# Performance work log

Measured on AMD Instinct MI355X. Metric: run time of the kernel, lower is better.

Reference implementation:

```python
import jax, jax.numpy as jnp
import numpy as np
from jax import lax

B, C, H, W = 4, 256, 64, 64
C8 = C // 8


def _conv1x1(x, w, b):
    # x: (B,C,H,W), w: (O,C) -> (B,O,H,W)
    return jnp.einsum('bchw,oc->bohw', x, w) + b[None, :, None, None]


def setup_inputs() -> dict:
    key = jax.random.key(0)
    ks = jax.random.split(key, 9)
    s1 = 1.0 / np.sqrt(C)          # fan-in scale for 1x1 convs
    sf = 1.0 / np.sqrt(2 * C * 9)  # fan-in scale for 3x3 conv
    return {
        'front_x':     jax.random.normal(ks[0], (B, C, H, W), jnp.float32),
        'cross_x':     jax.random.normal(ks[1], (B, C, H, W), jnp.float32),
        'front_x_hat': jax.random.normal(ks[2], (B, C, H, W), jnp.float32),
        'Wq': jax.random.normal(ks[3], (C8, C), jnp.float32) * s1,
        'bq': jnp.zeros((C8,), jnp.float32),
        'Wk': jax.random.normal(ks[4], (C8, C), jnp.float32) * s1,
        'bk': jnp.zeros((C8,), jnp.float32),
        'Wv': jax.random.normal(ks[5], (C, C), jnp.float32) * s1,
        'bv': jnp.zeros((C,), jnp.float32),
        'Wf': jax.random.normal(ks[6], (C, 2 * C, 3, 3), jnp.float32) * sf,
        'bf': jnp.zeros((C,), jnp.float32),
    }


def reference(front_x, cross_x, front_x_hat, Wq, bq, Wk, bk, Wv, bv, Wf, bf):
    b, c, h, w = front_x.shape
    hw = h * w
    # projections -> (B, C/8, HW)
    q = _conv1x1(cross_x, Wq, bq).reshape(b, -1, hw)
    k = _conv1x1(front_x, Wk, bk).reshape(b, -1, hw)
    # energy[b,i,j] = <key_i, query_j>  (B, HW, HW)
    energy = jnp.einsum('bci,bcj->bij', k, q)
    front_star = jnp.max(energy, axis=1)     # (B, HW) best key score per query
    front_arg = jnp.argmax(energy, axis=1)   # (B, HW) best key index per query
    # value projection and hard gather of best-matching value per position
    v = _conv1x1(front_x_hat, Wv, bv).reshape(b, c, hw)
    T = jnp.take_along_axis(v, front_arg[:, None, :], axis=2).reshape(b, c, h, w)
    S = front_star.reshape(b, 1, h, w)
    cat = jnp.concatenate([front_x, T], axis=1)  # (B, 2C, H, W)
    res = lax.conv_general_dilated(
        cat, Wf, window_strides=(1, 1), padding='SAME',
        dimension_numbers=('NCHW', 'OIHW', 'NCHW')) + bf[None, :, None, None]
    return front_x + res * S
```

## Files before the change

### kernel.cpp

```cpp
#include <hip/hip_runtime.h>

#define Bn 4
#define Cn 256
#define C8 32
#define Hn 64
#define Wn 64
#define HWn 4096
#define PADR 80
#define ROWS (HWn + 2 * PADR)
#define MARGIN 6e-3f

typedef __bf16 bf16x8 __attribute__((ext_vector_type(8)));
typedef float floatx4 __attribute__((ext_vector_type(4)));
typedef unsigned short u16x8 __attribute__((ext_vector_type(8)));

__device__ __forceinline__ unsigned short f2bf(float f) {
  union { float f; unsigned int u; } c; c.f = f;
  unsigned int u = c.u;
  return (unsigned short)((u + 0x7FFFu + ((u >> 16) & 1u)) >> 16);
}
__device__ __forceinline__ float bf2f(unsigned short h) {
  union { unsigned int u; float f; } c; c.u = ((unsigned int)h) << 16;
  return c.f;
}
__device__ __forceinline__ void gl_lds16(const void* g, void* l) {
  __builtin_amdgcn_global_load_lds(
      (__attribute__((address_space(1))) void*)(uintptr_t)g,
      (__attribute__((address_space(3))) void*)(uintptr_t)l, 16, 0, 0);
}

__global__ void prep_w(const float* __restrict__ Wq, const float* __restrict__ Wk,
                       const float* __restrict__ Wv, const float* __restrict__ Wf,
                       float* __restrict__ Wqf, float* __restrict__ Wkf,
                       unsigned short* __restrict__ Wvb, unsigned short* __restrict__ Wfb,
                       int* __restrict__ cnt) {
  size_t t = (size_t)blockIdx.x * 256 + threadIdx.x;
  if (t == 0) cnt[0] = 0;
  if (t < 8192) {
    int o = (int)(t / 256), c = (int)(t % 256);
    Wqf[(size_t)c * 32 + o] = Wq[t];
    Wkf[(size_t)c * 32 + o] = Wk[t];
  }
  if (t < 65536) Wvb[t] = f2bf(Wv[t]);
  if (t < (size_t)9 * 256 * 512) {
    int tap = (int)(t / (256 * 512));
    int rem = (int)(t % (256 * 512));
    int o = rem / 512, ci = rem % 512;
    Wfb[t] = f2bf(Wf[((size_t)o * 512 + ci) * 9 + tap]);
  }
}

__global__ __launch_bounds__(1024) void proj_qk(
    const float* __restrict__ cross_x, const float* __restrict__ front_x,
    const float* __restrict__ Wqf, const float* __restrict__ bq,
    const float* __restrict__ Wkf, const float* __restrict__ bk,
    float* __restrict__ qf, float* __restrict__ kf,
    unsigned short* __restrict__ qhi, unsigned short* __restrict__ qlo,
    unsigned short* __restrict__ khi, unsigned short* __restrict__ klo) {
  int tid = threadIdx.x;
  int lane = tid & 63, wv = tid >> 6;
  int slice = wv & 3;
  int chunk = wv >> 2;
  int j = blockIdx.x * 64 + lane;
  int b = blockIdx.y;
  int z = blockIdx.z;
  const float* x = (z == 0) ? cross_x : front_x;
  const float* Wg = (z == 0) ? Wqf : Wkf;
  const float* bd = (z == 0) ? bq : bk;
  float* outp = (z == 0) ? qf : kf;
  unsigned short* hip_ = (z == 0) ? qhi : khi;
  unsigned short* lop_ = (z == 0) ? qlo : klo;
  int o0 = slice * 8;
  int c0 = chunk * 64;

  __shared__ __align__(16) float Wl[8192];
  __shared__ float part[3 * 4 * 8 * 64];

  for (int u = tid; u < 8192; u += 1024) Wl[u] = Wg[u];
  __syncthreads();

  const float* xb = x + (size_t)b * Cn * HWn + j;
  floatx4 a0 = (floatx4)0.0f, a1 = (floatx4)0.0f;
#pragma unroll 16
  for (int c = c0; c < c0 + 64; ++c) {
    float xv = xb[(size_t)c * HWn];
    floatx4 wa = *reinterpret_cast<const floatx4*>(&Wl[c * 32 + o0]);
    floatx4 wb = *reinterpret_cast<const floatx4*>(&Wl[c * 32 + o0 + 4]);
    a0 += wa * xv;
    a1 += wb * xv;
  }
  if (chunk > 0) {
    float* dst = &part[(((chunk - 1) * 4 + slice) * 8) * 64];
#pragma unroll
    for (int o = 0; o < 4; ++o) { dst[o * 64 + lane] = a0[o]; dst[(o + 4) * 64 + lane] = a1[o]; }
  }
  __syncthreads();
  if (chunk != 0) return;
#pragma unroll
  for (int q = 0; q < 3; ++q) {
    const float* src = &part[((q * 4 + slice) * 8) * 64];
#pragma unroll
    for (int o = 0; o < 4; ++o) { a0[o] += src[o * 64 + lane]; a1[o] += src[(o + 4) * 64 + lane]; }
  }
  float acc[8];
#pragma unroll
  for (int o = 0; o < 4; ++o) { acc[o] = a0[o] + bd[o0 + o]; acc[o + 4] = a1[o] + bd[o0 + 4 + o]; }

  float* op = outp + ((size_t)b * HWn + j) * C8 + o0;
  u16x8 hv, lv;
#pragma unroll
  for (int o = 0; o < 8; ++o) {
    op[o] = acc[o];
    unsigned short h = f2bf(acc[o]);
    hv[o] = h;
    lv[o] = f2bf(acc[o] - bf2f(h));
  }
  *reinterpret_cast<u16x8*>(hip_ + ((size_t)b * HWn + j) * C8 + o0) = hv;
  *reinterpret_cast<u16x8*>(lop_ + ((size_t)b * HWn + j) * C8 + o0) = lv;
}

__global__ __launch_bounds__(1024) void energy_approx(
    const unsigned short* __restrict__ khi, const unsigned short* __restrict__ klo,
    const unsigned short* __restrict__ qhi, const unsigned short* __restrict__ qlo,
    float* __restrict__ star, int* __restrict__ argb,
    int* __restrict__ cnt, int* __restrict__ list) {
  int b = blockIdx.y;
  int j0 = blockIdx.x * 32;
  int tid = threadIdx.x;
  int lane = tid & 63, wv = tid >> 6;
  int lm = lane & 15, lq = lane >> 4;

  __shared__ float bv1S[16][32];
  __shared__ int   bi1S[16][32];
  __shared__ float bv2S[16][32];

  bf16x8 qh[2], ql[2];
#pragma unroll
  for (int s = 0; s < 2; ++s) {
    int j = j0 + s * 16 + lm;
    qh[s] = *reinterpret_cast<const bf16x8*>(qhi + ((size_t)b * HWn + j) * 32 + lq * 8);
    ql[s] = *reinterpret_cast<const bf16x8*>(qlo + ((size_t)b * HWn + j) * 32 + lq * 8);
  }
  const unsigned short* kh_base = khi + (size_t)b * HWn * 32 + lq * 8;
  const unsigned short* kl_base = klo + (size_t)b * HWn * 32 + lq * 8;

  float b1[2], b2[2];
#pragma unroll
  for (int s = 0; s < 2; ++s) { b1[s] = -3.0e38f; b2[s] = -3.0e38f; }

  int ibase = wv * 256;
#pragma unroll 4
  for (int it = 0; it < 16; ++it) {
    int i0 = ibase + it * 16;
    bf16x8 ah = *reinterpret_cast<const bf16x8*>(kh_base + (size_t)(i0 + lm) * 32);
    bf16x8 al = *reinterpret_cast<const bf16x8*>(kl_base + (size_t)(i0 + lm) * 32);
#pragma unroll
    for (int s = 0; s < 2; ++s) {
      floatx4 acc = (floatx4)0.0f;
      acc = __builtin_amdgcn_mfma_f32_16x16x32_bf16(ah, qh[s], acc, 0, 0, 0);
      acc = __builtin_amdgcn_mfma_f32_16x16x32_bf16(ah, ql[s], acc, 0, 0, 0);
      acc = __builtin_amdgcn_mfma_f32_16x16x32_bf16(al, qh[s], acc, 0, 0, 0);
#pragma unroll
      for (int r = 0; r < 4; ++r) {
        unsigned code = (unsigned)(it * 4 + r);
        union { float f; unsigned u; } cv; cv.f = acc[r];
        cv.u = (cv.u & ~63u) | code;
        float vp = cv.f;
        b2[s] = __builtin_amdgcn_fmed3f(vp, b1[s], b2[s]);
        b1[s] = fmaxf(b1[s], vp);
      }
    }
  }
  int i1[2];
#pragma unroll
  for (int s = 0; s < 2; ++s) {
    union { float f; unsigned u; } cv; cv.f = b1[s];
    unsigned code = cv.u & 63u;
    i1[s] = ibase + (int)(code >> 2) * 16 + lq * 4 + (int)(code & 3u);
  }
#pragma unroll
  for (int s = 0; s < 2; ++s) {
#pragma unroll
    for (int m = 16; m <= 32; m <<= 1) {
      float ob1 = __shfl_xor(b1[s], m, 64);
      int oi1 = __shfl_xor(i1[s], m, 64);
      float ob2 = __shfl_xor(b2[s], m, 64);
      float c2;
      if (ob1 > b1[s] || (ob1 == b1[s] && oi1 < i1[s])) {
        c2 = fmaxf(b1[s], ob2);
        b1[s] = ob1; i1[s] = oi1;
      } else {
        c2 = fmaxf(ob1, b2[s]);
      }
      b2[s] = c2;
    }
    if (lq == 0) {
      bv1S[wv][s * 16 + lm] = b1[s];
      bi1S[wv][s * 16 + lm] = i1[s];
      bv2S[wv][s * 16 + lm] = b2[s];
    }
  }
  __syncthreads();
  if (tid < 32) {
    float B1 = bv1S[0][tid];
    int I1 = bi1S[0][tid];
    float B2 = bv2S[0][tid];
#pragma unroll
    for (int w = 1; w < 16; ++w) {
      float v1 = bv1S[w][tid];
      int ii = bi1S[w][tid];
      float v2 = bv2S[w][tid];
      if (v1 > B1) { B2 = fmaxf(B1, v2); B1 = v1; I1 = ii; }
      else B2 = fmaxf(B2, v1);
    }
    size_t o = (size_t)b * HWn + j0 + tid;
    union { float f; unsigned u; } cs; cs.f = B1;
    cs.u &= ~63u;
    star[o] = cs.f;
    argb[o] = I1;
    if (B1 - B2 < MARGIN) {
      int slot = atomicAdd(cnt, 1);
      list[slot] = (b << 12) | (j0 + (int)tid);
    }
  }
}

__global__ __launch_bounds__(256) void recheck(
    const float* __restrict__ qf, const float* __restrict__ kf,
    const int* __restrict__ cnt, const int* __restrict__ list,
    float* __restrict__ star, int* __restrict__ argb) {
  __shared__ double bvS[4];
  __shared__ int biS[4];
  int n = cnt[0];
  int tid = threadIdx.x;
  int lane = tid & 63, wv = tid >> 6;
  for (int idx = blockIdx.x; idx < n; idx += gridDim.x) {
    int e = list[idx];
    int b = e >> 12, j = e & 4095;
    const float* qp = qf + ((size_t)b * HWn + j) * 32;
    double qj[32];
#pragma unroll
    for (int o = 0; o < 32; ++o) qj[o] = (double)qp[o];
    double best = -1.0e300;
    int bi = 1 << 30;
    for (int i = tid; i < HWn; i += 256) {
      const float* kp = kf + ((size_t)b * HWn + i) * 32;
      double s = 0.0;
#pragma unroll
      for (int o = 0; o < 32; ++o) s += (double)kp[o] * qj[o];
      if (s > best) { best = s; bi = i; }
    }
#pragma unroll
    for (int m = 1; m < 64; m <<= 1) {
      double ob = __shfl_xor(best, m, 64);
      int oi = __shfl_xor(bi, m, 64);
      if (ob > best || (ob == best && oi < bi)) { best = ob; bi = oi; }
    }
    if (lane == 0) { bvS[wv] = best; biS[wv] = bi; }
    __syncthreads();
    if (tid == 0) {
#pragma unroll
      for (int w = 1; w < 4; ++w) {
        if (bvS[w] > best || (bvS[w] == best && biS[w] < bi)) {
          best = bvS[w]; bi = biS[w];
        }
      }
      star[(size_t)b * HWn + j] = (float)best;
      argb[(size_t)b * HWn + j] = bi;
    }
    __syncthreads();
  }
}

__global__ __launch_bounds__(256) void cat_fx(
    const float* __restrict__ fx, const float* __restrict__ fxh,
    unsigned short* __restrict__ catC, unsigned short* __restrict__ xht) {
  int j0 = blockIdx.x * 64;
  int ci0 = blockIdx.y * 64;
  int b = blockIdx.z >> 1;
  int which = blockIdx.z & 1;
  int tid = threadIdx.x;
  __shared__ unsigned short tile[64][66];

  const float* src = (which == 0) ? fx : fxh;
  for (int u = tid; u < 4096; u += 256) {
    int cl = u >> 6, hw_l = u & 63;
    tile[cl][hw_l] = f2bf(src[((size_t)(b * Cn + ci0 + cl)) * HWn + j0 + hw_l]);
  }
  __syncthreads();
  if (which == 0) {
    for (int u = tid; u < 4096; u += 256) {
      int hw_l = u >> 6, cl = u & 63;
      catC[((size_t)b * ROWS + PADR + j0 + hw_l) * 512 + ci0 + cl] = tile[cl][hw_l];
    }
  } else {
    for (int u = tid; u < 4096; u += 256) {
      int hw_l = u >> 6, cl = u & 63;
      xht[((size_t)b * HWn + j0 + hw_l) * 256 + ci0 + cl] = tile[cl][hw_l];
    }
  }
}

__global__ __launch_bounds__(256) void proj_v_mfma(
    const unsigned short* __restrict__ xht, const unsigned short* __restrict__ Wvb,
    const float* __restrict__ bv, unsigned short* __restrict__ vbf) {
  int m0 = blockIdx.x * 128;
  int o0 = blockIdx.y * 128;
  int b = blockIdx.z;
  int tid = threadIdx.x;
  int lane = tid & 63, wv = tid >> 6;
  int wm = wv >> 1, wn = wv & 1;
  int lm = lane & 15, lq = lane >> 4;

  __shared__ __align__(16) unsigned short AS[128 * 32];
  __shared__ __align__(16) unsigned short BS[128 * 32];
  __shared__ __align__(16) unsigned short TS[128 * 136];

  floatx4 acc[4][4];
#pragma unroll
  for (int im = 0; im < 4; ++im)
#pragma unroll
    for (int in = 0; in < 4; ++in) acc[im][in] = (floatx4)0.0f;

  const int srow = lane >> 2;
  const int soff = (((lane & 3) ^ ((lane >> 3) & 3)) * 8);
  const int sa = (lq ^ ((lm >> 1) & 3)) * 8;
  const unsigned short* ag = Wvb + (size_t)o0 * 256;
  const unsigned short* bg = xht + ((size_t)b * HWn + m0) * 256;

  for (int kc = 0; kc < 256; kc += 32) {
    __syncthreads();
#pragma unroll
    for (int i = 0; i < 2; ++i) {
      int r0 = wv * 32 + i * 16;
      gl_lds16(ag + ((size_t)(r0 + srow)) * 256 + kc + soff, &AS[r0 * 32]);
      gl_lds16(bg + ((size_t)(r0 + srow)) * 256 + kc + soff, &BS[r0 * 32]);
    }
    __syncthreads();

    bf16x8 afr[4];
#pragma unroll
    for (int im = 0; im < 4; ++im)
      afr[im] = *reinterpret_cast<const bf16x8*>(
          &AS[(wm * 64 + im * 16 + lm) * 32 + sa]);
#pragma unroll
    for (int in = 0; in < 4; ++in) {
      bf16x8 bfr = *reinterpret_cast<const bf16x8*>(
          &BS[(wn * 64 + in * 16 + lm) * 32 + sa]);
#pragma unroll
      for (int im = 0; im < 4; ++im)
        acc[im][in] = __builtin_amdgcn_mfma_f32_16x16x32_bf16(
            afr[im], bfr, acc[im][in], 0, 0, 0);
    }
  }

  __syncthreads();
#pragma unroll
  for (int in = 0; in < 4; ++in) {
    int pl = wn * 64 + in * 16 + lm;
#pragma unroll
    for (int im = 0; im < 4; ++im) {
#pragma unroll
      for (int r = 0; r < 4; ++r) {
        int ol = wm * 64 + im * 16 + lq * 4 + r;
        TS[pl * 136 + ol] = f2bf(acc[im][in][r] + bv[o0 + ol]);
      }
    }
  }
  __syncthreads();
  for (int idx = tid; idx < 128 * 16; idx += 256) {
    int p = idx >> 4, ch = idx & 15;
    u16x8 val = *reinterpret_cast<const u16x8*>(&TS[p * 136 + ch * 8]);
    *reinterpret_cast<u16x8*>(
        &vbf[((size_t)b * HWn + m0 + p) * 256 + o0 + ch * 8]) = val;
  }
}

__global__ __launch_bounds__(256) void gather_cat(
    const unsigned short* __restrict__ vbf, const int* __restrict__ argb,
    unsigned short* __restrict__ catC) {
  int b = blockIdx.y;
  int tid = threadIdx.x;
  if (blockIdx.x == 16) {
    for (int u = tid; u < 2 * PADR * 512; u += 256) {
      int r = u >> 9;
      int rr = (r < PADR) ? r : (HWn + r);
      catC[((size_t)b * ROWS + rr) * 512 + (u & 511)] = 0;
    }
    return;
  }
  __shared__ int ajS[256];
  int j0 = blockIdx.x * 256;
  ajS[tid] = argb[(size_t)b * HWn + j0 + tid];
  __syncthreads();
#pragma unroll 4
  for (int u = tid; u < 256 * 32; u += 256) {
    int pl = u >> 5, ch = u & 31;
    int aj = ajS[pl];
    u16x8 val = *reinterpret_cast<const u16x8*>(
        &vbf[((size_t)b * HWn + aj) * 256 + ch * 8]);
    *reinterpret_cast<u16x8*>(
        &catC[((size_t)b * ROWS + PADR + j0 + pl) * 512 + 256 + ch * 8]) = val;
  }
}

__global__ __launch_bounds__(256) void conv_mfma(
    const unsigned short* __restrict__ catC, const unsigned short* __restrict__ Wfb,
    unsigned short* __restrict__ Pg) {
  int m0 = blockIdx.x * 128;
  int o0 = blockIdx.y * 128;
  int bz = blockIdx.z;
  int b = bz / 3, g = bz % 3;
  int dy = g - 1;
  int tid = threadIdx.x;
  int lane = tid & 63;
  int wv = tid >> 6;
  int wm = wv >> 1, wn = wv & 1;
  int lm = lane & 15, lq = lane >> 4;
  const bool lane_first = (lm == 0);
  const bool lane_last = (lm == 15);

  __shared__ __align__(16) unsigned short AS[3 * 128 * 32];
  __shared__ __align__(16) unsigned short BS[144 * 32];

  floatx4 acc[4][4];
#pragma unroll
  for (int im = 0; im < 4; ++im)
#pragma unroll
    for (int in = 0; in < 4; ++in) acc[im][in] = (floatx4)0.0f;

  const int srow = lane >> 2;
  const int soff = (((lane & 3) ^ ((lane >> 3) & 3)) * 8);
  const int sa = (lq ^ ((lm >> 1) & 3)) * 8;
  const unsigned short* bg =
      catC + ((size_t)b * ROWS + PADR + m0 + dy * 64 - 1) * 512;
  const unsigned short* ag = Wfb + ((size_t)(g * 3) * 256 + o0) * 512;

  for (int kc = 0; kc < 512; kc += 32) {
    __syncthreads();
    if (wv < 3) {
      const unsigned short* at = ag + (size_t)wv * 256 * 512;
#pragma unroll
      for (int s = 0; s < 8; ++s)
        gl_lds16(at + ((size_t)(s * 16 + srow)) * 512 + kc + soff,
                 &AS[(wv * 128 + s * 16) * 32]);
    } else {
#pragma unroll
      for (int s = 0; s < 9; ++s)
        gl_lds16(bg + ((size_t)(s * 16 + srow)) * 512 + kc + soff,
                 &BS[(s * 16) * 32]);
    }
    __syncthreads();

#pragma unroll
    for (int t = 0; t < 3; ++t) {
      bf16x8 afr[4];
#pragma unroll
      for (int im = 0; im < 4; ++im)
        afr[im] = *reinterpret_cast<const bf16x8*>(
            &AS[(t * 128 + wm * 64 + im * 16 + lm) * 32 + sa]);
#pragma unroll
      for (int in = 0; in < 4; ++in) {
        int u = wn * 64 + in * 16 + lm + t;
        int sb = (lq ^ ((u >> 1) & 3)) * 8;
        u16x8 braw = *reinterpret_cast<const u16x8*>(&BS[u * 32 + sb]);
        if ((t == 0 && in == 0 && lane_first) ||
            (t == 2 && in == 3 && lane_last))
          braw = (u16x8)(unsigned short)0;
        union { u16x8 u8; bf16x8 h; } cvt; cvt.u8 = braw;
#pragma unroll
        for (int im = 0; im < 4; ++im)
          acc[im][in] = __builtin_amdgcn_mfma_f32_16x16x32_bf16(
              afr[im], cvt.h, acc[im][in], 0, 0, 0);
      }
    }
  }

  unsigned short* P = Pg + ((size_t)(g * Bn + b) * Cn) * HWn;
#pragma unroll
  for (int in = 0; in < 4; ++in) {
    int p = m0 + wn * 64 + in * 16 + lm;
#pragma unroll
    for (int im = 0; im < 4; ++im) {
      int ob = o0 + wm * 64 + im * 16 + lq * 4;
#pragma unroll
      for (int r = 0; r < 4; ++r)
        P[(size_t)(ob + r) * HWn + p] = f2bf(acc[im][in][r]);
    }
  }
}

__global__ __launch_bounds__(256) void combine(
    const unsigned short* __restrict__ Pg, const float* __restrict__ fx,
    const float* __restrict__ bf, const float* __restrict__ star,
    float* __restrict__ out) {
  size_t e = ((size_t)blockIdx.x * 256 + threadIdx.x) * 8;
  int p = (int)(e & 4095);
  int bo = (int)(e >> 12);
  int o = bo & 255, b = bo >> 8;
  const size_t gs = (size_t)Bn * Cn * HWn;
  u16x8 q0 = *reinterpret_cast<const u16x8*>(Pg + e);
  u16x8 q1 = *reinterpret_cast<const u16x8*>(Pg + gs + e);
  u16x8 q2 = *reinterpret_cast<const u16x8*>(Pg + 2 * gs + e);
  float bias = bf[o];
  const float* sp = star + (size_t)b * HWn + p;
  const float* fp = fx + e;
  float* op = out + e;
#pragma unroll
  for (int h = 0; h < 2; ++h) {
    floatx4 s = *reinterpret_cast<const floatx4*>(sp + h * 4);
    floatx4 f = *reinterpret_cast<const floatx4*>(fp + h * 4);
    floatx4 r;
#pragma unroll
    for (int i = 0; i < 4; ++i) {
      int k = h * 4 + i;
      float a = bf2f(q0[k]) + bf2f(q1[k]) + bf2f(q2[k]);
      r[i] = f[i] + (a + bias) * s[i];
    }
    *reinterpret_cast<floatx4*>(op + h * 4) = r;
  }
}

extern "C" void kernel_launch(void* const* d_in, const int* in_sizes, int n_in,
                              void* d_out, int out_size, void* d_ws, size_t ws_size,
                              hipStream_t stream) {
  const float* front_x   = (const float*)d_in[0];
  const float* cross_x   = (const float*)d_in[1];
  const float* front_hat = (const float*)d_in[2];
  const float* Wq = (const float*)d_in[3];
  const float* bq = (const float*)d_in[4];
  const float* Wk = (const float*)d_in[5];
  const float* bk = (const float*)d_in[6];
  const float* Wv = (const float*)d_in[7];
  const float* bv = (const float*)d_in[8];
  const float* Wf = (const float*)d_in[9];
  const float* bf = (const float*)d_in[10];
  float* out = (float*)d_out;

  char* ws = (char*)d_ws;
  size_t off = 0;
  auto alloc = [&](size_t bytes) -> void* {
    void* p = (void*)(ws + off);
    off += (bytes + 255) & ~(size_t)255;
    return p;
  };
  float* Wqf = (float*)alloc(8192 * sizeof(float));
  float* Wkf = (float*)alloc(8192 * sizeof(float));
  unsigned short* Wvb = (unsigned short*)alloc(65536 * sizeof(unsigned short));
  unsigned short* Wfb = (unsigned short*)alloc((size_t)9 * 256 * 512 * sizeof(unsigned short));
  float* qf  = (float*)alloc((size_t)Bn * HWn * C8 * sizeof(float));
  float* kf  = (float*)alloc((size_t)Bn * HWn * C8 * sizeof(float));
  unsigned short* qhi = (unsigned short*)alloc((size_t)Bn * HWn * C8 * 2);
  unsigned short* qlo = (unsigned short*)alloc((size_t)Bn * HWn * C8 * 2);
  unsigned short* khi = (unsigned short*)alloc((size_t)Bn * HWn * C8 * 2);
  unsigned short* klo = (unsigned short*)alloc((size_t)Bn * HWn * C8 * 2);
  float*  star = (float*)alloc((size_t)Bn * HWn * sizeof(float));
  int*    argb = (int*)alloc((size_t)Bn * HWn * sizeof(int));
  int*    cnt  = (int*)alloc(256);
  int*    list = (int*)alloc((size_t)Bn * HWn * sizeof(int));
  unsigned short* xht = (unsigned short*)alloc((size_t)Bn * HWn * 256 * 2);
  unsigned short* vbf = (unsigned short*)alloc((size_t)Bn * HWn * 256 * 2);
  unsigned short* catC = (unsigned short*)alloc((size_t)Bn * ROWS * 512 * sizeof(unsigned short));
  unsigned short* Pg = (unsigned short*)alloc((size_t)3 * Bn * Cn * HWn * 2);

  prep_w<<<dim3((9 * 256 * 512 + 255) / 256), dim3(256), 0, stream>>>(
      Wq, Wk, Wv, Wf, Wqf, Wkf, Wvb, Wfb, cnt);

  proj_qk<<<dim3(HWn / 64, Bn, 2), dim3(1024), 0, stream>>>(
      cross_x, front_x, Wqf, bq, Wkf, bk, qf, kf, qhi, qlo, khi, klo);

  energy_approx<<<dim3(HWn / 32, Bn), dim3(1024), 0, stream>>>(
      khi, klo, qhi, qlo, star, argb, cnt, list);

  recheck<<<dim3(256), dim3(256), 0, stream>>>(qf, kf, cnt, list, star, argb);

  cat_fx<<<dim3(HWn / 64, Cn / 64, Bn * 2), dim3(256), 0, stream>>>(
      front_x, front_hat, catC, xht);

  proj_v_mfma<<<dim3(HWn / 128, Cn / 128, Bn), dim3(256), 0, stream>>>(
      xht, Wvb, bv, vbf);

  gather_cat<<<dim3(HWn / 256 + 1, Bn), dim3(256), 0, stream>>>(vbf, argb, catC);

  conv_mfma<<<dim3(HWn / 128, Cn / 128, Bn * 3), dim3(256), 0, stream>>>(
      catC, Wfb, Pg);

  combine<<<dim3((Bn * Cn * HWn / 8) / 256), dim3(256), 0, stream>>>(
      Pg, front_x, bf, star, out);
}
```

Baseline: 242.8 us.

## Double-buffer LDS staging in value projection and conv MFMA kernels

Both MFMA GEMM kernels (value projection and 3x3 conv) now keep two LDS buffers. The next K-chunk is issued to one buffer while MFMAs consume the other, which removes one barrier per iteration and hides global-to-LDS latency. In the projection kernel the epilogue transpose tile is unioned with the staging buffers to limit LDS growth. The conv kernel's LDS use doubles, which may lower occupancy.

```diff
diff --git a/kernel.cpp b/kernel.cpp
--- a/kernel.cpp
+++ b/kernel.cpp
@@ -312,9 +312,11 @@
   int wm = wv >> 1, wn = wv & 1;
   int lm = lane & 15, lq = lane >> 4;
 
-  __shared__ __align__(16) unsigned short AS[128 * 32];
-  __shared__ __align__(16) unsigned short BS[128 * 32];
-  __shared__ __align__(16) unsigned short TS[128 * 136];
+  union SMu {
+    struct { unsigned short A[2][128 * 32]; unsigned short B[2][128 * 32]; } st;
+    unsigned short TS[128 * 136];
+  };
+  __shared__ __align__(16) SMu sm;
 
   floatx4 acc[4][4];
 #pragma unroll
@@ -328,33 +330,42 @@
   const unsigned short* ag = Wvb + (size_t)o0 * 256;
   const unsigned short* bg = xht + ((size_t)b * HWn + m0) * 256;
 
-  for (int kc = 0; kc < 256; kc += 32) {
-    __syncthreads();
+  auto STAGE = [&](unsigned short* Ab, unsigned short* Bb, int kc) {
 #pragma unroll
     for (int i = 0; i < 2; ++i) {
       int r0 = wv * 32 + i * 16;
-      gl_lds16(ag + ((size_t)(r0 + srow)) * 256 + kc + soff, &AS[r0 * 32]);
-      gl_lds16(bg + ((size_t)(r0 + srow)) * 256 + kc + soff, &BS[r0 * 32]);
-    }
-    __syncthreads();
-
+      gl_lds16(ag + ((size_t)(r0 + srow)) * 256 + kc + soff, &Ab[r0 * 32]);
+      gl_lds16(bg + ((size_t)(r0 + srow)) * 256 + kc + soff, &Bb[r0 * 32]);
+    }
+  };
+  auto COMPUTE = [&](const unsigned short* Ab, const unsigned short* Bb) {
     bf16x8 afr[4];
 #pragma unroll
     for (int im = 0; im < 4; ++im)
       afr[im] = *reinterpret_cast<const bf16x8*>(
-          &AS[(wm * 64 + im * 16 + lm) * 32 + sa]);
+          &Ab[(wm * 64 + im * 16 + lm) * 32 + sa]);
 #pragma unroll
     for (int in = 0; in < 4; ++in) {
       bf16x8 bfr = *reinterpret_cast<const bf16x8*>(
-          &BS[(wn * 64 + in * 16 + lm) * 32 + sa]);
+          &Bb[(wn * 64 + in * 16 + lm) * 32 + sa]);
 #pragma unroll
       for (int im = 0; im < 4; ++im)
         acc[im][in] = __builtin_amdgcn_mfma_f32_16x16x32_bf16(
             afr[im], bfr, acc[im][in], 0, 0, 0);
     }
-  }
-
-  __syncthreads();
+  };
+
+  STAGE(sm.st.A[0], sm.st.B[0], 0);
+  __syncthreads();
+  for (int kci = 0; kci < 8; kci += 2) {
+    if (kci < 7) STAGE(sm.st.A[1], sm.st.B[1], (kci + 1) * 32);
+    COMPUTE(sm.st.A[0], sm.st.B[0]);
+    __syncthreads();
+    if (kci < 6) STAGE(sm.st.A[0], sm.st.B[0], (kci + 2) * 32);
+    COMPUTE(sm.st.A[1], sm.st.B[1]);
+    __syncthreads();
+  }
+
 #pragma unroll
   for (int in = 0; in < 4; ++in) {
     int pl = wn * 64 + in * 16 + lm;
@@ -363,14 +374,14 @@
 #pragma unroll
       for (int r = 0; r < 4; ++r) {
         int ol = wm * 64 + im * 16 + lq * 4 + r;
-        TS[pl * 136 + ol] = f2bf(acc[im][in][r] + bv[o0 + ol]);
+        sm.TS[pl * 136 + ol] = f2bf(acc[im][in][r] + bv[o0 + ol]);
       }
     }
   }
   __syncthreads();
   for (int idx = tid; idx < 128 * 16; idx += 256) {
     int p = idx >> 4, ch = idx & 15;
-    u16x8 val = *reinterpret_cast<const u16x8*>(&TS[p * 136 + ch * 8]);
+    u16x8 val = *reinterpret_cast<const u16x8*>(&sm.TS[p * 136 + ch * 8]);
     *reinterpret_cast<u16x8*>(
         &vbf[((size_t)b * HWn + m0 + p) * 256 + o0 + ch * 8]) = val;
   }
@@ -420,8 +431,8 @@
   const bool lane_first = (lm == 0);
   const bool lane_last = (lm == 15);
 
-  __shared__ __align__(16) unsigned short AS[3 * 128 * 32];
-  __shared__ __align__(16) unsigned short BS[144 * 32];
+  __shared__ __align__(16) unsigned short AS[2][3 * 128 * 32];
+  __shared__ __align__(16) unsigned short BS[2][144 * 32];
 
   floatx4 acc[4][4];
 #pragma unroll
@@ -436,34 +447,33 @@
       catC + ((size_t)b * ROWS + PADR + m0 + dy * 64 - 1) * 512;
   const unsigned short* ag = Wfb + ((size_t)(g * 3) * 256 + o0) * 512;
 
-  for (int kc = 0; kc < 512; kc += 32) {
-    __syncthreads();
+  auto STAGE = [&](unsigned short* ASb, unsigned short* BSb, int kc) {
     if (wv < 3) {
       const unsigned short* at = ag + (size_t)wv * 256 * 512;
 #pragma unroll
       for (int s = 0; s < 8; ++s)
         gl_lds16(at + ((size_t)(s * 16 + srow)) * 512 + kc + soff,
-                 &AS[(wv * 128 + s * 16) * 32]);
+                 &ASb[(wv * 128 + s * 16) * 32]);
     } else {
 #pragma unroll
       for (int s = 0; s < 9; ++s)
         gl_lds16(bg + ((size_t)(s * 16 + srow)) * 512 + kc + soff,
-                 &BS[(s * 16) * 32]);
-    }
-    __syncthreads();
-
+                 &BSb[(s * 16) * 32]);
+    }
+  };
+  auto COMPUTE = [&](const unsigned short* ASb, const unsigned short* BSb) {
 #pragma unroll
     for (int t = 0; t < 3; ++t) {
       bf16x8 afr[4];
 #pragma unroll
       for (int im = 0; im < 4; ++im)
         afr[im] = *reinterpret_cast<const bf16x8*>(
-            &AS[(t * 128 + wm * 64 + im * 16 + lm) * 32 + sa]);
+            &ASb[(t * 128 + wm * 64 + im * 16 + lm) * 32 + sa]);
 #pragma unroll
       for (int in = 0; in < 4; ++in) {
         int u = wn * 64 + in * 16 + lm + t;
         int sb = (lq ^ ((u >> 1) & 3)) * 8;
-        u16x8 braw = *reinterpret_cast<const u16x8*>(&BS[u * 32 + sb]);
+        u16x8 braw = *reinterpret_cast<const u16x8*>(&BSb[u * 32 + sb]);
         if ((t == 0 && in == 0 && lane_first) ||
             (t == 2 && in == 3 && lane_last))
           braw = (u16x8)(unsigned short)0;
@@ -474,6 +484,17 @@
               afr[im], cvt.h, acc[im][in], 0, 0, 0);
       }
     }
+  };
+
+  STAGE(AS[0], BS[0], 0);
+  __syncthreads();
+  for (int kci = 0; kci < 16; kci += 2) {
+    if (kci < 15) STAGE(AS[1], BS[1], (kci + 1) * 32);
+    COMPUTE(AS[0], BS[0]);
+    __syncthreads();
+    if (kci < 14) STAGE(AS[0], BS[0], (kci + 2) * 32);
+    COMPUTE(AS[1], BS[1]);
+    __syncthreads();
   }
 
   unsigned short* P = Pg + ((size_t)(g * Bn + b) * Cn) * HWn;
```

Measured after the change: 240.6 us. About the same (-0.9%).
